# Performance work log

Hardware: AMD Instinct MI355X
Metric: run time of the kernel (lower is better)

## Reference

```python
import jax, jax.numpy as jnp
import numpy as np

N_CODES = 1024
D = 128
BETA = 0.25


def setup_inputs() -> dict:
    key = jax.random.key(0)
    k1, k2 = jax.random.split(key)
    z = jax.random.normal(k1, (8, D, 4096), dtype=jnp.float32)  # (B, D, T)
    # nn.init.uniform_(codebook.weight, -1/n_codes, 1/n_codes)
    codebook = jax.random.uniform(
        k2, (N_CODES, D), dtype=jnp.float32,
        minval=-1.0 / N_CODES, maxval=1.0 / N_CODES)
    return {"z": z, "codebook": codebook}


def reference(z, codebook):
    B, D_, T = z.shape
    z_t = jnp.transpose(z, (0, 2, 1))           # (B, T, D)
    flat = z_t.reshape(B * T, D_)               # (BT, D)
    dist = (jnp.sum(flat * flat, axis=1, keepdims=True)
            - 2.0 * flat @ codebook.T
            + jnp.sum(codebook * codebook, axis=1)[None, :])
    codes = jnp.argmin(dist, axis=1)            # (BT,)
    z_q = codebook[codes].reshape(B, T, D_)     # (B, T, D)
    commit = jnp.mean((z_t - jax.lax.stop_gradient(z_q)) ** 2)
    codebk = jnp.mean((z_q - jax.lax.stop_gradient(z_t)) ** 2)
    loss = codebk + BETA * commit
    # straight-through estimator
    z_q_st = z_t + jax.lax.stop_gradient(z_q - z_t)
    z_q_out = jnp.transpose(z_q_st, (0, 2, 1))  # (B, D, T)
    return (z_q_out, codes.reshape(B, T), loss,
            dist.reshape(B, T, codebook.shape[0]))
```

## Files before the change

kernel.cpp:

```cpp
#include <hip/hip_runtime.h>

typedef __attribute__((ext_vector_type(8))) short short8;
typedef __attribute__((ext_vector_type(4))) float f32x4;

namespace {
constexpr long long OFF_CODES = 4194304;
constexpr long long OFF_LOSS  = 4227072;
constexpr long long OFF_DIST  = 4227073;
constexpr float EPS = 5e-4f;
constexpr size_t WS_LACC = 0;
constexpr size_t WS_SCF  = 1024;
constexpr size_t WS_SZF  = 8192;
constexpr size_t WS_FLAG = 139264;
constexpr size_t WS_CBF  = 270336;
}

__device__ __forceinline__ unsigned short bf_rne(float v) {
  unsigned int u = __float_as_uint(v);
  unsigned int r = u + 0x7FFFu + ((u >> 16) & 1u);
  return (unsigned short)(r >> 16);
}

__global__ __launch_bounds__(256) void vq_cbfrag(
    const float* __restrict__ cb, unsigned short* __restrict__ cbf,
    float* __restrict__ scf, double* lacc)
{
  __shared__ double pn[4][16];
  const int g = blockIdx.x;
  const int tid = threadIdx.x;
  const int ks = tid >> 6, l = tid & 63, lg = l >> 4, lj = l & 15;
  const float* src = cb + (size_t)(g * 16 + lj) * 128 + ks * 32 + lg * 8;
  double s = 0.0;
  short8 h;
#pragma unroll
  for (int e = 0; e < 8; ++e) {
    float v = src[e];
    float q = v * v;
    s += (double)q;
    h[e] = (short)bf_rne(v);
  }
  *reinterpret_cast<short8*>(cbf + (size_t)g * 2048 + (size_t)tid * 8) = h;
  s += __shfl_xor(s, 16);
  s += __shfl_xor(s, 32);
  if (lg == 0) pn[ks][lj] = s;
  __syncthreads();
  if (tid < 16)
    scf[g * 16 + tid] = (float)(pn[0][tid] + pn[1][tid] + pn[2][tid] + pn[3][tid]);
  if (blockIdx.x == 0 && tid == 0) *lacc = 0.0;
}

__global__ __launch_bounds__(256) void vq_szf(
    const float* __restrict__ z, float* __restrict__ szf)
{
  __shared__ double pn[64][4];
  const int tid = threadIdx.x;
  const int R0 = blockIdx.x * 64;
  const int b = R0 >> 12, t0 = R0 & 4095;
  const int t = tid & 63, dg = tid >> 6;
  const float* zp = z + (size_t)b * 524288 + (size_t)dg * 32 * 4096 + t0 + t;
  double s = 0.0;
#pragma unroll
  for (int d = 0; d < 32; ++d) {
    float v = zp[(size_t)d * 4096];
    float q = v * v;
    s += (double)q;
  }
  pn[t][dg] = s;
  __syncthreads();
  if (tid < 64)
    szf[R0 + tid] = (float)(pn[tid][0] + pn[tid][1] + pn[tid][2] + pn[tid][3]);
}

__global__ __launch_bounds__(256, 4) void vq_main(
    const float* __restrict__ z, const unsigned short* __restrict__ cbf,
    const float* __restrict__ scf, const float* __restrict__ szf,
    unsigned int* __restrict__ flags, float* __restrict__ out)
{
  __shared__ __align__(16) unsigned short zh[32 * 136];
  __shared__ float scfl[1024];
  __shared__ float szl[32];
  __shared__ float rm1[4][32], rm2[4][32];
  __shared__ int   ri1[4][32];

  const int tid = threadIdx.x;
  const int R0 = blockIdx.x * 32;
  const int b = R0 >> 12, t0 = R0 & 4095;
  const float* zb = z + (size_t)b * 524288;

#pragma unroll
  for (int k = 0; k < 4; ++k) scfl[k * 256 + tid] = scf[k * 256 + tid];
  if (tid < 32) szl[tid] = szf[R0 + tid];

  {
    int t = tid & 31;
#pragma unroll
    for (int k = 0; k < 16; ++k) {
      int d = k * 8 + (tid >> 5);
      zh[t * 136 + d] = bf_rne(zb[(size_t)d * 4096 + t0 + t]);
    }
  }
  __syncthreads();

  const int w = tid >> 6, l = tid & 63, lj = l & 15, lg = l >> 4;

  short8 Ah[2][4];
#pragma unroll
  for (int tt = 0; tt < 2; ++tt)
#pragma unroll
    for (int ks = 0; ks < 4; ++ks)
      Ah[tt][ks] = *reinterpret_cast<const short8*>(
          &zh[(tt * 16 + lj) * 136 + ks * 32 + lg * 8]);
  float szr[2][4];
#pragma unroll
  for (int tt = 0; tt < 2; ++tt)
#pragma unroll
    for (int r = 0; r < 4; ++r) szr[tt][r] = szl[tt * 16 + lg * 4 + r];

  float m1[8], m2[8]; int i1[8];
#pragma unroll
  for (int s = 0; s < 8; ++s) { m1[s] = 3.4e38f; m2[s] = 3.4e38f; i1[s] = 0; }

  const unsigned short* pwave = cbf + (size_t)w * 16 * 2048 + (size_t)l * 8;

#pragma unroll 1
  for (int q = 0; q < 4; ++q) {
    f32x4 acc[2][4];
#pragma unroll
    for (int u = 0; u < 4; ++u) {
      acc[0][u] = (f32x4){0.f, 0.f, 0.f, 0.f};
      acc[1][u] = (f32x4){0.f, 0.f, 0.f, 0.f};
      const unsigned short* pg = pwave + (size_t)(q * 4 + u) * 2048;
#pragma unroll
      for (int ks = 0; ks < 4; ++ks) {
        short8 bh = *reinterpret_cast<const short8*>(pg + ks * 512);
        acc[0][u] = __builtin_amdgcn_mfma_f32_16x16x32_bf16(Ah[0][ks], bh, acc[0][u], 0, 0, 0);
        acc[1][u] = __builtin_amdgcn_mfma_f32_16x16x32_bf16(Ah[1][ks], bh, acc[1][u], 0, 0, 0);
      }
    }
#pragma unroll
    for (int u = 0; u < 4; ++u) {
      const int jj = w * 256 + (q * 4 + u) * 16 + lj;
      const float sc = scfl[jj];
#pragma unroll
      for (int tt = 0; tt < 2; ++tt)
#pragma unroll
        for (int r = 0; r < 4; ++r) {
          float dv = (szr[tt][r] - 2.0f * acc[tt][u][r]) + sc;
          const int s = tt * 4 + r;
          bool lt1 = dv < m1[s];
          float o1 = m1[s];
          m2[s] = lt1 ? o1 : fminf(m2[s], dv);
          m1[s] = lt1 ? dv : o1;
          i1[s] = lt1 ? jj : i1[s];
          out[OFF_DIST + (size_t)(R0 + tt * 16 + lg * 4 + r) * 1024 + jj] = dv;
        }
    }
  }

#pragma unroll
  for (int s = 0; s < 8; ++s) {
    float a1 = m1[s]; int ai = i1[s]; float a2 = m2[s];
#pragma unroll
    for (int msk = 1; msk <= 8; msk <<= 1) {
      float b1 = __shfl_xor(a1, msk);
      int   bi = __shfl_xor(ai, msk);
      float b2 = __shfl_xor(a2, msk);
      bool keep = (a1 < b1) || (a1 == b1 && ai < bi);
      float lose = keep ? b1 : a1;
      a2 = fminf(fminf(a2, b2), lose);
      ai = keep ? ai : bi;
      a1 = keep ? a1 : b1;
    }
    if (lj == 0) {
      int t = (s >> 2) * 16 + lg * 4 + (s & 3);
      rm1[w][t] = a1; ri1[w][t] = ai; rm2[w][t] = a2;
    }
  }
  __syncthreads();
  if (tid < 32) {
    float f1 = rm1[0][tid]; int fi = ri1[0][tid]; float f2 = rm2[0][tid];
#pragma unroll
    for (int ww = 1; ww < 4; ++ww) {
      float b1 = rm1[ww][tid]; int bi = ri1[ww][tid]; float b2 = rm2[ww][tid];
      bool keep = (f1 < b1) || (f1 == b1 && fi < bi);
      float lose = keep ? b1 : f1;
      f2 = fminf(fminf(f2, b2), lose);
      fi = keep ? fi : bi;
      f1 = keep ? f1 : b1;
    }
    int R = R0 + tid;
    out[OFF_CODES + R] = (float)fi;
    flags[R] = (f2 - f1 <= EPS) ? 1u : 0u;
  }
}

__global__ __launch_bounds__(256) void vq_refine(
    const float* __restrict__ z, const float* __restrict__ cb,
    const float* __restrict__ scf, const float* __restrict__ szf,
    const unsigned int* __restrict__ flags, float* __restrict__ out)
{
  const int w = threadIdx.x >> 6, l = threadIdx.x & 63;
  const int R = blockIdx.x * 4 + w;
  if (!flags[R]) return;
  const int b = R >> 12, t = R & 4095;

  const float* drow = out + OFF_DIST + (size_t)R * 1024;
  float v[16];
#pragma unroll
  for (int k = 0; k < 16; ++k) v[k] = drow[k * 64 + l];
  float mn = 3.4e38f;
#pragma unroll
  for (int k = 0; k < 16; ++k) mn = fminf(mn, v[k]);
#pragma unroll
  for (int msk = 1; msk <= 32; msk <<= 1) mn = fminf(mn, __shfl_xor(mn, msk));
  const float thresh = mn + EPS;

  const double zd0 = (double)z[(size_t)b * 524288 + (size_t)l * 4096 + t];
  const double zd1 = (double)z[(size_t)b * 524288 + (size_t)(l + 64) * 4096 + t];
  const float szv = szf[R];

  float bestv = 3.4e38f; int bestj = 1 << 30;
#pragma unroll
  for (int k = 0; k < 16; ++k) {
    unsigned long long msk = __ballot(v[k] <= thresh);
    while (msk) {
      int s = __ffsll((unsigned long long)msk) - 1;
      msk &= msk - 1;
      int jc = k * 64 + s;
      float c0 = cb[(size_t)jc * 128 + l];
      float c1 = cb[(size_t)jc * 128 + 64 + l];
      double m = zd0 * (double)c0 + zd1 * (double)c1;
#pragma unroll
      for (int mm = 1; mm <= 32; mm <<= 1) m += __shfl_xor(m, mm);
      float m32 = (float)m;
      float dvex = (szv - 2.0f * m32) + scf[jc];
      if (dvex < bestv || (dvex == bestv && jc < bestj)) { bestv = dvex; bestj = jc; }
    }
  }
  if (l == 0) out[OFF_CODES + R] = (float)bestj;
}

__global__ __launch_bounds__(256) void vq_out_kernel(
    const float* __restrict__ z, const float* __restrict__ cb,
    float* __restrict__ out, double* __restrict__ lacc)
{
  __shared__ int ci[128];
  __shared__ float cq[128][129];
  __shared__ double lw[4];
  const int tid = threadIdx.x;
  const int b  = blockIdx.x >> 5;
  const int t0 = (blockIdx.x & 31) * 128;
  const int R0 = b * 4096 + t0;
  if (tid < 128) ci[tid] = (int)out[OFF_CODES + R0 + tid];
  __syncthreads();
  for (int r = 0; r < 128; r += 2) {
    int row = r + (tid >> 7);
    int d = tid & 127;
    cq[row][d] = cb[(size_t)ci[row] * 128 + d];
  }
  __syncthreads();
  double ls = 0.0;
  for (int dp = 0; dp < 128; dp += 2) {
    int d = dp + (tid >> 7);
    int t = tid & 127;
    size_t o = (size_t)b * 524288 + (size_t)d * 4096 + t0 + t;
    float zv = z[o];
    float q = cq[t][d];
    out[o] = zv + (q - zv);
    double dd = (double)q - (double)zv;
    ls += dd * dd;
  }
#pragma unroll
  for (int msk = 1; msk <= 32; msk <<= 1) ls += __shfl_xor(ls, msk);
  if ((tid & 63) == 0) lw[tid >> 6] = ls;
  __syncthreads();
  if (tid == 0) atomicAdd(lacc, lw[0] + lw[1] + lw[2] + lw[3]);
}

__global__ void vq_fin(const double* lacc, float* out) {
  if (threadIdx.x == 0 && blockIdx.x == 0)
    out[OFF_LOSS] = (float)(*lacc * (1.25 / 4194304.0));
}

extern "C" void kernel_launch(void* const* d_in, const int* in_sizes, int n_in,
                              void* d_out, int out_size, void* d_ws, size_t ws_size,
                              hipStream_t stream) {
  const float* z  = (const float*)d_in[0];
  const float* cb = (const float*)d_in[1];
  float* out = (float*)d_out;
  char* ws = (char*)d_ws;
  double* lacc = (double*)(ws + WS_LACC);
  float* scf = (float*)(ws + WS_SCF);
  float* szf = (float*)(ws + WS_SZF);
  unsigned int* flags = (unsigned int*)(ws + WS_FLAG);
  unsigned short* cbf = (unsigned short*)(ws + WS_CBF);

  vq_cbfrag<<<64, 256, 0, stream>>>(cb, cbf, scf, lacc);
  vq_szf<<<512, 256, 0, stream>>>(z, szf);
  vq_main<<<1024, 256, 0, stream>>>(z, cbf, scf, szf, flags, out);
  vq_refine<<<8192, 256, 0, stream>>>(z, cb, scf, szf, flags, out);
  vq_out_kernel<<<256, 256, 0, stream>>>(z, cb, out, lacc);
  vq_fin<<<1, 64, 0, stream>>>(lacc, out);
}
```

Measured before the change: 79.23 us.

## Fuse z-norm and output/loss stages into main VQ kernel, stage dist writes via LDS

Computes the per-row squared norm of z inside vq_main while loading z, which removes the separate vq_szf kernel. Keeps the z tile in registers so vq_main can gather the chosen codebook rows and write the straight-through output and loss itself, removing vq_out_kernel and its second read of z. The refine kernel now patches the output and adjusts the loss by a delta only for rows whose code changes. The distance tile is staged through shared memory and written as coalesced float4 rows. In exchange shared memory grows, occupancy drops from 4 to 3 blocks, and each q iteration gains two extra barriers.

Result: slower. 106.2 us (+34.0%).

```diff
diff --git a/kernel.cpp b/kernel.cpp
--- a/kernel.cpp
+++ b/kernel.cpp
@@ -49,38 +49,21 @@
   if (blockIdx.x == 0 && tid == 0) *lacc = 0.0;
 }
 
-__global__ __launch_bounds__(256) void vq_szf(
-    const float* __restrict__ z, float* __restrict__ szf)
-{
-  __shared__ double pn[64][4];
-  const int tid = threadIdx.x;
-  const int R0 = blockIdx.x * 64;
-  const int b = R0 >> 12, t0 = R0 & 4095;
-  const int t = tid & 63, dg = tid >> 6;
-  const float* zp = z + (size_t)b * 524288 + (size_t)dg * 32 * 4096 + t0 + t;
-  double s = 0.0;
-#pragma unroll
-  for (int d = 0; d < 32; ++d) {
-    float v = zp[(size_t)d * 4096];
-    float q = v * v;
-    s += (double)q;
-  }
-  pn[t][dg] = s;
-  __syncthreads();
-  if (tid < 64)
-    szf[R0 + tid] = (float)(pn[tid][0] + pn[tid][1] + pn[tid][2] + pn[tid][3]);
-}
-
-__global__ __launch_bounds__(256, 4) void vq_main(
+__global__ __launch_bounds__(256, 3) void vq_main(
     const float* __restrict__ z, const unsigned short* __restrict__ cbf,
-    const float* __restrict__ scf, const float* __restrict__ szf,
-    unsigned int* __restrict__ flags, float* __restrict__ out)
+    const float* __restrict__ cb, const float* __restrict__ scf,
+    float* __restrict__ szf, unsigned int* __restrict__ flags,
+    float* __restrict__ out, double* __restrict__ lacc)
 {
   __shared__ __align__(16) unsigned short zh[32 * 136];
+  __shared__ __align__(16) float sd[32 * 272];
+  __shared__ double part[32][8];
+  __shared__ float szl[32];
   __shared__ float scfl[1024];
-  __shared__ float szl[32];
   __shared__ float rm1[4][32], rm2[4][32];
   __shared__ int   ri1[4][32];
+  __shared__ int   ci[32];
+  __shared__ double lw[4];
 
   const int tid = threadIdx.x;
   const int R0 = blockIdx.x * 32;
@@ -89,15 +72,30 @@
 
 #pragma unroll
   for (int k = 0; k < 4; ++k) scfl[k * 256 + tid] = scf[k * 256 + tid];
-  if (tid < 32) szl[tid] = szf[R0 + tid];
-
+
+  float zreg[16];
   {
-    int t = tid & 31;
+    double ps = 0.0;
+    const int t = tid & 31;
 #pragma unroll
     for (int k = 0; k < 16; ++k) {
       int d = k * 8 + (tid >> 5);
-      zh[t * 136 + d] = bf_rne(zb[(size_t)d * 4096 + t0 + t]);
-    }
+      float v = zb[(size_t)d * 4096 + t0 + t];
+      zreg[k] = v;
+      float q = v * v;
+      ps += (double)q;
+      zh[t * 136 + d] = bf_rne(v);
+    }
+    part[t][tid >> 5] = ps;
+  }
+  __syncthreads();
+  if (tid < 32) {
+    double s = 0.0;
+#pragma unroll
+    for (int g = 0; g < 8; ++g) s += part[tid][g];
+    float sz = (float)s;
+    szl[tid] = sz;
+    szf[R0 + tid] = sz;
   }
   __syncthreads();
 
@@ -121,6 +119,10 @@
   for (int s = 0; s < 8; ++s) { m1[s] = 3.4e38f; m2[s] = 3.4e38f; i1[s] = 0; }
 
   const unsigned short* pwave = cbf + (size_t)w * 16 * 2048 + (size_t)l * 8;
+
+  const int srow = (tid >> 1) & 31, sww = tid >> 6 >= 0 ? ((tid >> 1) >> 5) : 0;
+  const float* ssrc = sd + srow * 272 + sww * 68;
+  float* sgbase = out + OFF_DIST + (size_t)(R0 + srow) * 1024 + sww * 256;
 
 #pragma unroll 1
   for (int q = 0; q < 4; ++q) {
@@ -152,9 +154,27 @@
           m2[s] = lt1 ? o1 : fminf(m2[s], dv);
           m1[s] = lt1 ? dv : o1;
           i1[s] = lt1 ? jj : i1[s];
-          out[OFF_DIST + (size_t)(R0 + tt * 16 + lg * 4 + r) * 1024 + jj] = dv;
+          sd[(tt * 16 + lg * 4 + r) * 272 + w * 68 + 1 + u * 16 + lj] = dv;
         }
     }
+    __syncthreads();
+    {
+      float* gdst = sgbase + q * 64;
+      if ((tid & 1) == 0) {
+        gdst[0] = ssrc[1]; gdst[1] = ssrc[2]; gdst[2] = ssrc[3];
+#pragma unroll
+        for (int c = 0; c < 7; ++c)
+          *reinterpret_cast<float4*>(gdst + 3 + 4 * c) =
+              *reinterpret_cast<const float4*>(ssrc + 4 + 4 * c);
+      } else {
+#pragma unroll
+        for (int c = 7; c < 15; ++c)
+          *reinterpret_cast<float4*>(gdst + 3 + 4 * c) =
+              *reinterpret_cast<const float4*>(ssrc + 4 + 4 * c);
+        gdst[63] = ssrc[64];
+      }
+    }
+    __syncthreads();
   }
 
 #pragma unroll
@@ -191,13 +211,44 @@
     int R = R0 + tid;
     out[OFF_CODES + R] = (float)fi;
     flags[R] = (f2 - f1 <= EPS) ? 1u : 0u;
-  }
+    ci[tid] = fi;
+  }
+  __syncthreads();
+
+  {
+    const int row = tid >> 3, p = tid & 7;
+    const float* csrc = cb + (size_t)ci[row] * 128 + p * 16;
+#pragma unroll
+    for (int e = 0; e < 16; ++e) sd[row * 133 + p * 16 + e] = csrc[e];
+  }
+  __syncthreads();
+
+  double ls = 0.0;
+  {
+    const int t = tid & 31, dg = tid >> 5;
+    float* zq = out + (size_t)b * 524288 + t0 + t;
+#pragma unroll
+    for (int k = 0; k < 16; ++k) {
+      int d = k * 8 + dg;
+      float zv = zreg[k];
+      float qv = sd[t * 133 + d];
+      zq[(size_t)d * 4096] = zv + (qv - zv);
+      double dd = (double)qv - (double)zv;
+      ls += dd * dd;
+    }
+  }
+#pragma unroll
+  for (int msk = 1; msk <= 32; msk <<= 1) ls += __shfl_xor(ls, msk);
+  if ((tid & 63) == 0) lw[tid >> 6] = ls;
+  __syncthreads();
+  if (tid == 0) atomicAdd(lacc, lw[0] + lw[1] + lw[2] + lw[3]);
 }
 
 __global__ __launch_bounds__(256) void vq_refine(
     const float* __restrict__ z, const float* __restrict__ cb,
     const float* __restrict__ scf, const float* __restrict__ szf,
-    const unsigned int* __restrict__ flags, float* __restrict__ out)
+    const unsigned int* __restrict__ flags, float* __restrict__ out,
+    double* __restrict__ lacc)
 {
   const int w = threadIdx.x >> 6, l = threadIdx.x & 63;
   const int R = blockIdx.x * 4 + w;
@@ -215,8 +266,9 @@
   for (int msk = 1; msk <= 32; msk <<= 1) mn = fminf(mn, __shfl_xor(mn, msk));
   const float thresh = mn + EPS;
 
-  const double zd0 = (double)z[(size_t)b * 524288 + (size_t)l * 4096 + t];
-  const double zd1 = (double)z[(size_t)b * 524288 + (size_t)(l + 64) * 4096 + t];
+  const float zv0f = z[(size_t)b * 524288 + (size_t)l * 4096 + t];
+  const float zv1f = z[(size_t)b * 524288 + (size_t)(l + 64) * 4096 + t];
+  const double zd0 = (double)zv0f, zd1 = (double)zv1f;
   const float szv = szf[R];
 
   float bestv = 3.4e38f; int bestj = 1 << 30;
@@ -237,44 +289,24 @@
       if (dvex < bestv || (dvex == bestv && jc < bestj)) { bestv = dvex; bestj = jc; }
     }
   }
-  if (l == 0) out[OFF_CODES + R] = (float)bestj;
-}
-
-__global__ __launch_bounds__(256) void vq_out_kernel(
-    const float* __restrict__ z, const float* __restrict__ cb,
-    float* __restrict__ out, double* __restrict__ lacc)
-{
-  __shared__ int ci[128];
-  __shared__ float cq[128][129];
-  __shared__ double lw[4];
-  const int tid = threadIdx.x;
-  const int b  = blockIdx.x >> 5;
-  const int t0 = (blockIdx.x & 31) * 128;
-  const int R0 = b * 4096 + t0;
-  if (tid < 128) ci[tid] = (int)out[OFF_CODES + R0 + tid];
-  __syncthreads();
-  for (int r = 0; r < 128; r += 2) {
-    int row = r + (tid >> 7);
-    int d = tid & 127;
-    cq[row][d] = cb[(size_t)ci[row] * 128 + d];
-  }
-  __syncthreads();
-  double ls = 0.0;
-  for (int dp = 0; dp < 128; dp += 2) {
-    int d = dp + (tid >> 7);
-    int t = tid & 127;
-    size_t o = (size_t)b * 524288 + (size_t)d * 4096 + t0 + t;
-    float zv = z[o];
-    float q = cq[t][d];
-    out[o] = zv + (q - zv);
-    double dd = (double)q - (double)zv;
-    ls += dd * dd;
-  }
-#pragma unroll
-  for (int msk = 1; msk <= 32; msk <<= 1) ls += __shfl_xor(ls, msk);
-  if ((tid & 63) == 0) lw[tid >> 6] = ls;
-  __syncthreads();
-  if (tid == 0) atomicAdd(lacc, lw[0] + lw[1] + lw[2] + lw[3]);
+
+  const int fiOld = (int)out[OFF_CODES + R];
+  if (bestj != fiOld) {
+    if (l == 0) out[OFF_CODES + R] = (float)bestj;
+    float cn0 = cb[(size_t)bestj * 128 + l];
+    float cn1 = cb[(size_t)bestj * 128 + 64 + l];
+    float co0 = cb[(size_t)fiOld * 128 + l];
+    float co1 = cb[(size_t)fiOld * 128 + 64 + l];
+    float* zq = out + (size_t)b * 524288 + t;
+    zq[(size_t)l * 4096]        = zv0f + (cn0 - zv0f);
+    zq[(size_t)(l + 64) * 4096] = zv1f + (cn1 - zv1f);
+    double dn0 = (double)cn0 - zd0, dn1 = (double)cn1 - zd1;
+    double do0 = (double)co0 - zd0, do1 = (double)co1 - zd1;
+    double dl = dn0 * dn0 + dn1 * dn1 - do0 * do0 - do1 * do1;
+#pragma unroll
+    for (int mm = 1; mm <= 32; mm <<= 1) dl += __shfl_xor(dl, mm);
+    if (l == 0) atomicAdd(lacc, dl);
+  }
 }
 
 __global__ void vq_fin(const double* lacc, float* out) {
@@ -296,9 +328,7 @@
   unsigned short* cbf = (unsigned short*)(ws + WS_CBF);
 
   vq_cbfrag<<<64, 256, 0, stream>>>(cb, cbf, scf, lacc);
-  vq_szf<<<512, 256, 0, stream>>>(z, szf);
-  vq_main<<<1024, 256, 0, stream>>>(z, cbf, scf, szf, flags, out);
-  vq_refine<<<8192, 256, 0, stream>>>(z, cb, scf, szf, flags, out);
-  vq_out_kernel<<<256, 256, 0, stream>>>(z, cb, out, lacc);
+  vq_main<<<1024, 256, 0, stream>>>(z, cbf, cb, scf, szf, flags, out, lacc);
+  vq_refine<<<8192, 256, 0, stream>>>(z, cb, scf, szf, flags, out, lacc);
   vq_fin<<<1, 64, 0, stream>>>(lacc, out);
 }
```

## Swap MFMA operands so each lane owns codes contiguously and stores float4 distances

Applied to the files above, without the earlier changes.

Swaps the MFMA A/B operands so codebook fragments become the row operand and z rows the column operand. Each lane then holds four consecutive codes for a single row, so the distance values can be written as one 16-byte store instead of four scattered scalar stores. The per-lane argmin state shrinks from 8 rows to 2, and the cross-lane reduction uses xor masks 16/32 instead of 1..8. Accumulators are now consumed per u-step, which lowers register pressure but makes the scf reads from LDS per-element rather than per-column.

Measured after the change: 79.87 us. About the same (+0.8%).

```diff
diff --git a/kernel.cpp b/kernel.cpp
--- a/kernel.cpp
+++ b/kernel.cpp
@@ -79,8 +79,8 @@
   __shared__ __align__(16) unsigned short zh[32 * 136];
   __shared__ float scfl[1024];
   __shared__ float szl[32];
-  __shared__ float rm1[4][32], rm2[4][32];
-  __shared__ int   ri1[4][32];
+  __shared__ float rm1[4][2][16], rm2[4][2][16];
+  __shared__ int   ri1[4][2][16];
 
   const int tid = threadIdx.x;
   const int R0 = blockIdx.x * 32;
@@ -103,65 +103,60 @@
 
   const int w = tid >> 6, l = tid & 63, lj = l & 15, lg = l >> 4;
 
-  short8 Ah[2][4];
-#pragma unroll
-  for (int tt = 0; tt < 2; ++tt)
+  short8 Bz[2][4];
+#pragma unroll
+  for (int th = 0; th < 2; ++th)
 #pragma unroll
     for (int ks = 0; ks < 4; ++ks)
-      Ah[tt][ks] = *reinterpret_cast<const short8*>(
-          &zh[(tt * 16 + lj) * 136 + ks * 32 + lg * 8]);
-  float szr[2][4];
-#pragma unroll
-  for (int tt = 0; tt < 2; ++tt)
-#pragma unroll
-    for (int r = 0; r < 4; ++r) szr[tt][r] = szl[tt * 16 + lg * 4 + r];
-
-  float m1[8], m2[8]; int i1[8];
-#pragma unroll
-  for (int s = 0; s < 8; ++s) { m1[s] = 3.4e38f; m2[s] = 3.4e38f; i1[s] = 0; }
+      Bz[th][ks] = *reinterpret_cast<const short8*>(
+          &zh[(th * 16 + lj) * 136 + ks * 32 + lg * 8]);
+  const float szt[2] = { szl[lj], szl[16 + lj] };
+
+  float m1[2], m2[2]; int i1[2];
+#pragma unroll
+  for (int s = 0; s < 2; ++s) { m1[s] = 3.4e38f; m2[s] = 3.4e38f; i1[s] = 0; }
 
   const unsigned short* pwave = cbf + (size_t)w * 16 * 2048 + (size_t)l * 8;
 
 #pragma unroll 1
   for (int q = 0; q < 4; ++q) {
-    f32x4 acc[2][4];
 #pragma unroll
     for (int u = 0; u < 4; ++u) {
-      acc[0][u] = (f32x4){0.f, 0.f, 0.f, 0.f};
-      acc[1][u] = (f32x4){0.f, 0.f, 0.f, 0.f};
       const unsigned short* pg = pwave + (size_t)(q * 4 + u) * 2048;
+      f32x4 acc0 = (f32x4){0.f, 0.f, 0.f, 0.f};
+      f32x4 acc1 = (f32x4){0.f, 0.f, 0.f, 0.f};
 #pragma unroll
       for (int ks = 0; ks < 4; ++ks) {
-        short8 bh = *reinterpret_cast<const short8*>(pg + ks * 512);
-        acc[0][u] = __builtin_amdgcn_mfma_f32_16x16x32_bf16(Ah[0][ks], bh, acc[0][u], 0, 0, 0);
-        acc[1][u] = __builtin_amdgcn_mfma_f32_16x16x32_bf16(Ah[1][ks], bh, acc[1][u], 0, 0, 0);
+        short8 af = *reinterpret_cast<const short8*>(pg + ks * 512);
+        acc0 = __builtin_amdgcn_mfma_f32_16x16x32_bf16(af, Bz[0][ks], acc0, 0, 0, 0);
+        acc1 = __builtin_amdgcn_mfma_f32_16x16x32_bf16(af, Bz[1][ks], acc1, 0, 0, 0);
       }
-    }
-#pragma unroll
-    for (int u = 0; u < 4; ++u) {
-      const int jj = w * 256 + (q * 4 + u) * 16 + lj;
-      const float sc = scfl[jj];
-#pragma unroll
-      for (int tt = 0; tt < 2; ++tt)
+      const int j0 = w * 256 + (q * 4 + u) * 16 + lg * 4;
+#pragma unroll
+      for (int th = 0; th < 2; ++th) {
+        f32x4 dvv;
 #pragma unroll
         for (int r = 0; r < 4; ++r) {
-          float dv = (szr[tt][r] - 2.0f * acc[tt][u][r]) + sc;
-          const int s = tt * 4 + r;
-          bool lt1 = dv < m1[s];
-          float o1 = m1[s];
-          m2[s] = lt1 ? o1 : fminf(m2[s], dv);
-          m1[s] = lt1 ? dv : o1;
-          i1[s] = lt1 ? jj : i1[s];
-          out[OFF_DIST + (size_t)(R0 + tt * 16 + lg * 4 + r) * 1024 + jj] = dv;
+          float m = (th == 0) ? acc0[r] : acc1[r];
+          float dv = (szt[th] - 2.0f * m) + scfl[j0 + r];
+          bool lt1 = dv < m1[th];
+          float o1 = m1[th];
+          m2[th] = lt1 ? o1 : fminf(m2[th], dv);
+          m1[th] = lt1 ? dv : o1;
+          i1[th] = lt1 ? (j0 + r) : i1[th];
+          dvv[r] = dv;
         }
-    }
-  }
-
-#pragma unroll
-  for (int s = 0; s < 8; ++s) {
-    float a1 = m1[s]; int ai = i1[s]; float a2 = m2[s];
-#pragma unroll
-    for (int msk = 1; msk <= 8; msk <<= 1) {
+        __builtin_memcpy(
+            out + OFF_DIST + (size_t)(R0 + th * 16 + lj) * 1024 + j0, &dvv, 16);
+      }
+    }
+  }
+
+#pragma unroll
+  for (int th = 0; th < 2; ++th) {
+    float a1 = m1[th]; int ai = i1[th]; float a2 = m2[th];
+#pragma unroll
+    for (int msk = 16; msk <= 32; msk <<= 1) {
       float b1 = __shfl_xor(a1, msk);
       int   bi = __shfl_xor(ai, msk);
       float b2 = __shfl_xor(a2, msk);
@@ -171,17 +166,15 @@
       ai = keep ? ai : bi;
       a1 = keep ? a1 : b1;
     }
-    if (lj == 0) {
-      int t = (s >> 2) * 16 + lg * 4 + (s & 3);
-      rm1[w][t] = a1; ri1[w][t] = ai; rm2[w][t] = a2;
-    }
+    if (lg == 0) { rm1[w][th][lj] = a1; ri1[w][th][lj] = ai; rm2[w][th][lj] = a2; }
   }
   __syncthreads();
   if (tid < 32) {
-    float f1 = rm1[0][tid]; int fi = ri1[0][tid]; float f2 = rm2[0][tid];
+    const int th = tid >> 4, ljj = tid & 15;
+    float f1 = rm1[0][th][ljj]; int fi = ri1[0][th][ljj]; float f2 = rm2[0][th][ljj];
 #pragma unroll
     for (int ww = 1; ww < 4; ++ww) {
-      float b1 = rm1[ww][tid]; int bi = ri1[ww][tid]; float b2 = rm2[ww][tid];
+      float b1 = rm1[ww][th][ljj]; int bi = ri1[ww][th][ljj]; float b2 = rm2[ww][th][ljj];
       bool keep = (f1 < b1) || (f1 == b1 && fi < bi);
       float lose = keep ? b1 : f1;
       f2 = fminf(fminf(f2, b2), lose);
```
